# Kernel tuning notes

Hardware: AMD Instinct MI355X
Metric: run time of the kernel (lower is better)

Reference implementation:

```python
import jax, jax.numpy as jnp
import numpy as np

TEMP = 0.1
GROUPS = 16
EPS = 1e-5
COS_EPS = 1e-8


def _encoder(x, conv_w, conv_b, gn_g, gn_b):
    # Conv2d(C,C,3,pad=1) -> GroupNorm(16,C) -> ReLU -> AdaptiveAvgPool2d(1) -> Flatten
    y = jax.lax.conv_general_dilated(
        x, conv_w, window_strides=(1, 1), padding='SAME',
        dimension_numbers=('NCHW', 'OIHW', 'NCHW')) + conv_b[None, :, None, None]
    B, C, H, W = y.shape
    yg = y.reshape(B, GROUPS, C // GROUPS, H, W)
    mu = yg.mean(axis=(2, 3, 4), keepdims=True)
    var = yg.var(axis=(2, 3, 4), keepdims=True)
    yn = ((yg - mu) * jax.lax.rsqrt(var + EPS)).reshape(B, C, H, W)
    y = yn * gn_g[None, :, None, None] + gn_b[None, :, None, None]
    y = jax.nn.relu(y)
    return y.mean(axis=(2, 3))  # [B, C]


def _projector(h, w1, b1, w2, b2, ln_g, ln_b):
    h = jax.nn.relu(h @ w1 + b1)
    h = h @ w2 + b2
    mu = h.mean(axis=-1, keepdims=True)
    var = h.var(axis=-1, keepdims=True)
    return (h - mu) * jax.lax.rsqrt(var + EPS) * ln_g + ln_b


def _predictor(z, w1, b1, w2, b2):
    return jax.nn.relu(z @ w1 + b1) @ w2 + b2


def _l2norm(z):
    n = jnp.sqrt(jnp.sum(z * z, axis=1, keepdims=True))
    return z / jnp.maximum(n, COS_EPS)


def _pair_loss(zi, zj, off_idx):
    # vectorized version of the nested-loop cosine-sim + cross-entropy (label 0)
    S = (_l2norm(zi) @ _l2norm(zj).T) / TEMP  # [B, B]
    pos = jnp.diagonal(S)                     # sim(i_k, j_k)
    neg = jnp.take_along_axis(S, off_idx, axis=1)  # [B, B-1], row k = S[k, l!=k]
    logits = jnp.concatenate([pos[:, None], neg], axis=1)
    return jnp.mean(jax.nn.logsumexp(logits, axis=1) - logits[:, 0])


def setup_inputs() -> dict:
    key = jax.random.key(0)
    ks = jax.random.split(key, 32)
    B, C, H, W, P = 256, 256, 16, 16, 128
    d = {}
    d['x_t2w'] = jax.random.normal(ks[0], (B, C, H, W), jnp.float32)
    d['x_t2f'] = jax.random.normal(ks[1], (B, C, H, W), jnp.float32)
    d['x_t1n'] = jax.random.normal(ks[2], (B, C, H, W), jnp.float32)
    i = 3
    for m in ('t2w', 't2f', 't1n'):
        d[f'conv_w_{m}'] = jax.random.normal(ks[i], (C, C, 3, 3), jnp.float32) * 0.02; i += 1
        d[f'conv_b_{m}'] = jnp.zeros((C,), jnp.float32)
        d[f'gn_g_{m}'] = jnp.ones((C,), jnp.float32)
        d[f'gn_b_{m}'] = jnp.zeros((C,), jnp.float32)
    d['proj_w1'] = jax.random.normal(ks[i], (C, C), jnp.float32) * 0.02; i += 1
    d['proj_b1'] = jnp.zeros((C,), jnp.float32)
    d['proj_w2'] = jax.random.normal(ks[i], (C, P), jnp.float32) * 0.02; i += 1
    d['proj_b2'] = jnp.zeros((P,), jnp.float32)
    d['ln_g'] = jnp.ones((P,), jnp.float32)
    d['ln_b'] = jnp.zeros((P,), jnp.float32)
    d['pred_w1'] = jax.random.normal(ks[i], (P, P), jnp.float32) * 0.02; i += 1
    d['pred_b1'] = jnp.zeros((P,), jnp.float32)
    d['pred_w2'] = jax.random.normal(ks[i], (P, P), jnp.float32) * 0.02; i += 1
    d['pred_b2'] = jnp.zeros((P,), jnp.float32)
    return d


def reference(x_t2w, x_t2f, x_t1n,
              conv_w_t2w, conv_b_t2w, gn_g_t2w, gn_b_t2w,
              conv_w_t2f, conv_b_t2f, gn_g_t2f, gn_b_t2f,
              conv_w_t1n, conv_b_t1n, gn_g_t1n, gn_b_t1n,
              proj_w1, proj_b1, proj_w2, proj_b2, ln_g, ln_b,
              pred_w1, pred_b1, pred_w2, pred_b2):
    xs = [x_t2w, x_t2f, x_t1n]
    enc_params = [(conv_w_t2w, conv_b_t2w, gn_g_t2w, gn_b_t2w),
                  (conv_w_t2f, conv_b_t2f, gn_g_t2f, gn_b_t2f),
                  (conv_w_t1n, conv_b_t1n, gn_g_t1n, gn_b_t1n)]
    encoded = [_encoder(x, *p) for x, p in zip(xs, enc_params)]
    projected = [_projector(e, proj_w1, proj_b1, proj_w2, proj_b2, ln_g, ln_b) for e in encoded]
    preds = [_predictor(z, pred_w1, pred_b1, pred_w2, pred_b2) for z in projected]

    B = projected[0].shape[0]
    off_idx = jnp.asarray(np.array([[l for l in range(B) if l != k] for k in range(B)],
                                    dtype=np.int32))
    pairs = [(0, 1), (0, 2), (1, 2)]
    loss = sum(_pair_loss(projected[i], projected[j], off_idx) for i, j in pairs) / len(pairs)

    return (jnp.stack(encoded), jnp.stack(projected), jnp.stack(preds), loss)
```

## Files before the change

kernel.cpp:

```cpp
#include <hip/hip_runtime.h>
#include <hip/hip_bf16.h>

typedef float f32x4 __attribute__((ext_vector_type(4)));
typedef __bf16 bf16x8 __attribute__((ext_vector_type(8)));
typedef unsigned short u16x8 __attribute__((ext_vector_type(8)));

#define GN_EPS 1e-5f
#define LN_EPS 1e-5f
#define COS_EPS_F 1e-8f

__device__ __forceinline__ unsigned short f2bf(float f) {
  unsigned int u = __builtin_bit_cast(unsigned int, f);
  u += 0x7fffu + ((u >> 16) & 1u);
  return (unsigned short)(u >> 16);
}

__global__ void transpose_kernel(const float* __restrict__ x0,
                                 const float* __restrict__ x1,
                                 const float* __restrict__ x2,
                                 unsigned short* __restrict__ xT,
                                 unsigned int strideElems, int mBase) {
  __shared__ float lds[64][129];
  int m = mBase + (blockIdx.x >> 11);
  int bid = blockIdx.x & 2047;
  const float* x = (m == 0) ? x0 : ((m == 1) ? x1 : x2);
  unsigned short* dst = xT + (unsigned int)(m - mBase) * strideElems;

  int hwt = bid & 3, cit = (bid >> 2) & 1, b = bid >> 3;
  int hw0 = hwt * 64, ci0 = cit * 128;
  int tid = threadIdx.x;

  int hwx = tid & 63, cy0 = tid >> 6;
  const float* xb = x + (b * 256 + ci0) * 256 + hw0;
  #pragma unroll 8
  for (int p = 0; p < 32; ++p) {
    int cy = cy0 + 4 * p;
    lds[hwx][cy] = xb[cy * 256 + hwx];
  }
  __syncthreads();

  int cp = tid & 63, hy0 = tid >> 6;
  unsigned int* outp = (unsigned int*)(dst + (b * 256 + hw0) * 256 + ci0);
  #pragma unroll 4
  for (int p = 0; p < 16; ++p) {
    int hy = hy0 + 4 * p;
    float lo = lds[hy][2 * cp];
    float hi = lds[hy][2 * cp + 1];
    unsigned int w = ((unsigned int)f2bf(hi) << 16) | f2bf(lo);
    outp[hy * 128 + cp] = w;
  }
}

__global__ void pack_kernel(const float* __restrict__ w0,
                            const float* __restrict__ w1,
                            const float* __restrict__ w2,
                            unsigned short* __restrict__ wp,
                            unsigned short* __restrict__ zerobuf) {
  int m = blockIdx.y;
  const float* w = (m == 0) ? w0 : ((m == 1) ? w1 : w2);
  int idx = blockIdx.x * 256 + threadIdx.x;
  if (m == 0 && blockIdx.x == 0 && threadIdx.x < 256) zerobuf[threadIdx.x] = 0;
  int ci = idx & 255;
  int rest = idx >> 8;
  int khw = rest % 9, co = rest / 9;
  wp[m * 589824 + idx] = f2bf(w[(co * 256 + ci) * 9 + khw]);
}

__device__ __forceinline__ void gl_lds16(const unsigned short* g, unsigned short* l) {
  __builtin_amdgcn_global_load_lds(
      (const __attribute__((address_space(1))) void*)g,
      (__attribute__((address_space(3))) void*)l, 16, 0, 0);
}

__launch_bounds__(512, 2)
__global__ void conv_gn_pool(const unsigned short* __restrict__ xT,
                             unsigned int xTstride,
                             const unsigned short* __restrict__ wp,
                             const unsigned short* __restrict__ zb,
                             const float* __restrict__ cb0, const float* __restrict__ cb1,
                             const float* __restrict__ cb2,
                             const float* __restrict__ gg0, const float* __restrict__ gg1,
                             const float* __restrict__ gg2,
                             const float* __restrict__ gb0, const float* __restrict__ gb1,
                             const float* __restrict__ gb2,
                             float* __restrict__ enc, int mBase) {
  __shared__ unsigned short Ab[4][8192];
  __shared__ unsigned short Bb[4][8192];
  __shared__ float gsum[16], gsq[16], pooled[256];

  int mm = mBase + (blockIdx.x >> 8);
  int bb = blockIdx.x & 255;
  int b = (bb & 7) * 32 + (bb >> 3);
  const float* cbias = (mm == 0) ? cb0 : ((mm == 1) ? cb1 : cb2);
  const float* gng   = (mm == 0) ? gg0 : ((mm == 1) ? gg1 : gg2);
  const float* gnb   = (mm == 0) ? gb0 : ((mm == 1) ? gb1 : gb2);

  int tid = threadIdx.x;
  int wid = tid >> 6, lane = tid & 63;
  int wr = wid >> 2, wc = wid & 3;
  int l15 = lane & 15, l4 = lane >> 4;

  if (tid < 16) { gsum[tid] = 0.f; gsq[tid] = 0.f; }
  if (tid < 256) pooled[tid] = 0.f;

  int s0 = tid, s1 = 512 + tid;
  int r0 = s0 >> 2, c0 = s0 & 3;
  int r1 = s1 >> 2, c1 = s1 & 3;
  int cs0 = (c0 ^ ((r0 >> 1) & 3)) * 8;
  int cs1 = (c1 ^ ((r1 >> 1) & 3)) * 8;
  int rh0 = r0 >> 4, rw0 = r0 & 15;
  int rh1 = r1 >> 4, rw1 = r1 & 15;

  const unsigned short* xb = xT + (unsigned int)(mm - mBase) * xTstride + b * 65536;
  const unsigned short* wpm = wp + mm * 589824;
  const unsigned short* bB0 = wpm + r0 * 2304 + cs0;
  const unsigned short* bB1 = wpm + r1 * 2304 + cs1;

  int kch = (l4 ^ ((l15 >> 1) & 3)) * 8;
  int base_af = (wr * 128 + l15) * 32 + kch;
  int base_bf = (wc * 64 + l15) * 32 + kch;

  f32x4 acc[8][4];
  #pragma unroll
  for (int i = 0; i < 8; ++i)
    #pragma unroll
    for (int j = 0; j < 4; ++j) acc[i][j] = (f32x4)(0.0f);

  #define STAGE_A(KC, KHW, BUF)                                                \
    {                                                                          \
      int kh_ = (KHW) / 3, kw_ = (KHW) % 3;                                    \
      int ci0_ = (KC) * 32;                                                    \
      unsigned short* dst_ = &Ab[(BUF)][0];                                    \
      int h0_ = rh0 + kh_ - 1, w0_ = rw0 + kw_ - 1;                            \
      const unsigned short* sA0 = ((unsigned)h0_ < 16u && (unsigned)w0_ < 16u) \
          ? xb + ((h0_ * 16 + w0_) * 256 + ci0_ + cs0) : zb;                   \
      gl_lds16(sA0, dst_ + s0 * 8);                                            \
      int h1_ = rh1 + kh_ - 1, w1_ = rw1 + kw_ - 1;                            \
      const unsigned short* sA1 = ((unsigned)h1_ < 16u && (unsigned)w1_ < 16u) \
          ? xb + ((h1_ * 16 + w1_) * 256 + ci0_ + cs1) : zb;                   \
      gl_lds16(sA1, dst_ + s1 * 8);                                            \
    }
  #define STAGE_B(KC, KHW, BUF)                                                \
    {                                                                          \
      int off_ = (KHW) * 256 + (KC) * 32;                                      \
      unsigned short* dst_ = &Bb[(BUF)][0];                                    \
      gl_lds16(bB0 + off_, dst_ + s0 * 8);                                     \
      gl_lds16(bB1 + off_, dst_ + s1 * 8);                                     \
    }

  #define TILE_COMPUTE(BUF)                                                    \
    {                                                                          \
      const unsigned short* Ap = &Ab[(BUF)][0];                                \
      const unsigned short* Bp = &Bb[(BUF)][0];                                \
      bf16x8 af[8], bfr[4];                                                    \
      _Pragma("unroll")                                                        \
      for (int j = 0; j < 8; ++j)                                              \
        af[j] = __builtin_bit_cast(bf16x8, *(const u16x8*)&Ap[base_af + j * 512]); \
      _Pragma("unroll")                                                        \
      for (int n = 0; n < 4; ++n)                                              \
        bfr[n] = __builtin_bit_cast(bf16x8, *(const u16x8*)&Bp[base_bf + n * 512]); \
      __builtin_amdgcn_s_setprio(1);                                           \
      _Pragma("unroll")                                                        \
      for (int j = 0; j < 8; ++j)                                              \
        _Pragma("unroll")                                                      \
        for (int n = 0; n < 4; ++n)                                            \
          acc[j][n] = __builtin_amdgcn_mfma_f32_16x16x32_bf16(af[j], bfr[n],   \
                                                              acc[j][n], 0, 0, 0); \
      __builtin_amdgcn_s_setprio(0);                                           \
    }

  STAGE_A(0, 0, 0); STAGE_B(0, 0, 0);
  STAGE_A(0, 1, 1); STAGE_B(0, 1, 1);
  STAGE_A(0, 2, 2); STAGE_B(0, 2, 2);
  asm volatile("s_waitcnt vmcnt(8)" ::: "memory");
  __builtin_amdgcn_s_barrier();

  for (int kc = 0; kc < 7; ++kc) {
    #pragma unroll
    for (int khw = 0; khw < 9; ++khw) {
      int buf = (kc + khw) & 3;
      int buf3 = (kc + khw + 3) & 3;
      if (khw <= 5) { STAGE_A(kc, khw + 3, buf3); STAGE_B(kc, khw + 3, buf3); }
      else          { STAGE_A(kc + 1, khw - 6, buf3); STAGE_B(kc + 1, khw - 6, buf3); }
      TILE_COMPUTE(buf);
      asm volatile("s_waitcnt vmcnt(8)" ::: "memory");
      __builtin_amdgcn_s_barrier();
    }
  }
  #pragma unroll
  for (int khw = 0; khw < 9; ++khw) {
    int buf = (7 + khw) & 3;
    int buf3 = (7 + khw + 3) & 3;
    if (khw <= 5) { STAGE_A(7, khw + 3, buf3); STAGE_B(7, khw + 3, buf3); }
    TILE_COMPUTE(buf);
    if (khw <= 5)      asm volatile("s_waitcnt vmcnt(8)" ::: "memory");
    else if (khw == 6) asm volatile("s_waitcnt vmcnt(4)" ::: "memory");
    else               asm volatile("s_waitcnt vmcnt(0)" ::: "memory");
    __builtin_amdgcn_s_barrier();
  }
  #undef STAGE_A
  #undef STAGE_B
  #undef TILE_COMPUTE

  float bias[4], ggv[4], gbv[4];
  #pragma unroll
  for (int nf = 0; nf < 4; ++nf) {
    int co = wc * 64 + nf * 16 + l15;
    bias[nf] = cbias[co]; ggv[nf] = gng[co]; gbv[nf] = gnb[co];
  }
  #pragma unroll
  for (int nf = 0; nf < 4; ++nf) {
    float s1 = 0.f, s2 = 0.f;
    #pragma unroll
    for (int mf = 0; mf < 8; ++mf)
      #pragma unroll
      for (int i = 0; i < 4; ++i) {
        float v = acc[mf][nf][i] + bias[nf];
        acc[mf][nf][i] = v;
        s1 += v; s2 += v * v;
      }
    #pragma unroll
    for (int d = 1; d < 64; d <<= 1) {
      s1 += __shfl_xor(s1, d);
      s2 += __shfl_xor(s2, d);
    }
    if (lane == 0) {
      atomicAdd(&gsum[wc * 4 + nf], s1);
      atomicAdd(&gsq[wc * 4 + nf], s2);
    }
  }
  __syncthreads();
  #pragma unroll
  for (int nf = 0; nf < 4; ++nf) {
    int g = wc * 4 + nf;
    float mean = gsum[g] * (1.f / 4096.f);
    float var = gsq[g] * (1.f / 4096.f) - mean * mean;
    float rs = rsqrtf(var + GN_EPS);
    float p = 0.f;
    #pragma unroll
    for (int mf = 0; mf < 8; ++mf)
      #pragma unroll
      for (int i = 0; i < 4; ++i) {
        float v = (acc[mf][nf][i] - mean) * rs * ggv[nf] + gbv[nf];
        p += fmaxf(v, 0.f);
      }
    p += __shfl_xor(p, 16);
    p += __shfl_xor(p, 32);
    if (lane < 16) atomicAdd(&pooled[wc * 64 + nf * 16 + l15], p);
  }
  __syncthreads();
  if (tid < 256)
    enc[mm * 65536 + b * 256 + tid] = pooled[tid] * (1.f / 256.f);
}

__global__ void proj_pred(const float* __restrict__ enc,
                          const float* __restrict__ w1, const float* __restrict__ b1,
                          const float* __restrict__ w2, const float* __restrict__ b2,
                          const float* __restrict__ lng, const float* __restrict__ lnb,
                          const float* __restrict__ pw1, const float* __restrict__ pb1,
                          const float* __restrict__ pw2, const float* __restrict__ pb2,
                          float* __restrict__ proj, float* __restrict__ pred,
                          float* __restrict__ znorm) {
  __shared__ float row[256], h1[256], zz[128], p1[128], red[2];
  int r = blockIdx.x, tid = threadIdx.x;
  row[tid] = enc[r * 256 + tid];
  __syncthreads();
  float a = 0.f;
  for (int k = 0; k < 256; ++k) a += row[k] * w1[k * 256 + tid];
  h1[tid] = fmaxf(a + b1[tid], 0.f);
  __syncthreads();
  if (tid < 128) {
    a = 0.f;
    for (int k = 0; k < 256; ++k) a += h1[k] * w2[k * 128 + tid];
    zz[tid] = a + b2[tid];
  }
  __syncthreads();
  if (tid == 0) {
    float m = 0.f;
    for (int k = 0; k < 128; ++k) m += zz[k];
    m *= (1.f / 128.f);
    float v = 0.f;
    for (int k = 0; k < 128; ++k) { float d = zz[k] - m; v += d * d; }
    red[0] = m;
    red[1] = rsqrtf(v * (1.f / 128.f) + LN_EPS);
  }
  __syncthreads();
  float zval = 0.f;
  if (tid < 128) {
    zval = (zz[tid] - red[0]) * red[1] * lng[tid] + lnb[tid];
    proj[r * 128 + tid] = zval;
  }
  __syncthreads();
  if (tid < 128) zz[tid] = zval;
  __syncthreads();
  if (tid == 0) {
    float s = 0.f;
    for (int k = 0; k < 128; ++k) s += zz[k] * zz[k];
    red[0] = 1.f / fmaxf(sqrtf(s), COS_EPS_F);
  }
  __syncthreads();
  if (tid < 128) {
    znorm[r * 128 + tid] = zz[tid] * red[0];
    a = 0.f;
    for (int k = 0; k < 128; ++k) a += zz[k] * pw1[k * 128 + tid];
    p1[tid] = fmaxf(a + pb1[tid], 0.f);
  }
  __syncthreads();
  if (tid < 128) {
    a = 0.f;
    for (int k = 0; k < 128; ++k) a += p1[k] * pw2[k * 128 + tid];
    pred[r * 128 + tid] = a + pb2[tid];
  }
}

__global__ void loss_kernel(const float* __restrict__ zn, float* __restrict__ part) {
  __shared__ float zi[128], sv[256], rbuf[256];
  int blk = blockIdx.x;
  int p = blk >> 8, k = blk & 255;
  int i = (p == 2) ? 1 : 0;
  int j = (p == 0) ? 1 : 2;
  int tid = threadIdx.x;
  if (tid < 128) zi[tid] = zn[(i * 256 + k) * 128 + tid];
  __syncthreads();
  const float4* zj = (const float4*)&zn[(j * 256 + tid) * 128];
  float s = 0.f;
  #pragma unroll 8
  for (int d = 0; d < 32; ++d) {
    float4 aq = *(const float4*)&zi[d * 4];
    float4 bq = zj[d];
    s += aq.x * bq.x + aq.y * bq.y + aq.z * bq.z + aq.w * bq.w;
  }
  s *= 10.0f;
  sv[tid] = s;
  rbuf[tid] = s;
  __syncthreads();
  for (int d = 128; d > 0; d >>= 1) {
    if (tid < d) rbuf[tid] = fmaxf(rbuf[tid], rbuf[tid + d]);
    __syncthreads();
  }
  float m = rbuf[0];
  __syncthreads();
  rbuf[tid] = expf(s - m);
  __syncthreads();
  for (int d = 128; d > 0; d >>= 1) {
    if (tid < d) rbuf[tid] += rbuf[tid + d];
    __syncthreads();
  }
  if (tid == 0) part[blk] = m + logf(rbuf[0]) - sv[k];
}

__global__ void finalize_loss(const float* __restrict__ part, float* __restrict__ out) {
  __shared__ float red[256];
  int tid = threadIdx.x;
  float s = 0.f;
  for (int idx = tid; idx < 768; idx += 256) s += part[idx];
  red[tid] = s;
  __syncthreads();
  for (int d = 128; d > 0; d >>= 1) {
    if (tid < d) red[tid] += red[tid + d];
    __syncthreads();
  }
  if (tid == 0) out[0] = red[0] * (1.f / 768.f);
}

extern "C" void kernel_launch(void* const* d_in, const int* in_sizes, int n_in,
                              void* d_out, int out_size, void* d_ws, size_t ws_size,
                              hipStream_t stream) {
  const float* x[3]  = {(const float*)d_in[0], (const float*)d_in[1], (const float*)d_in[2]};
  const float* cw[3] = {(const float*)d_in[3], (const float*)d_in[7], (const float*)d_in[11]};
  const float* cb[3] = {(const float*)d_in[4], (const float*)d_in[8], (const float*)d_in[12]};
  const float* gg[3] = {(const float*)d_in[5], (const float*)d_in[9], (const float*)d_in[13]};
  const float* gb[3] = {(const float*)d_in[6], (const float*)d_in[10], (const float*)d_in[14]};
  const float* p_w1 = (const float*)d_in[15];
  const float* p_b1 = (const float*)d_in[16];
  const float* p_w2 = (const float*)d_in[17];
  const float* p_b2 = (const float*)d_in[18];
  const float* ln_g = (const float*)d_in[19];
  const float* ln_b = (const float*)d_in[20];
  const float* q_w1 = (const float*)d_in[21];
  const float* q_b1 = (const float*)d_in[22];
  const float* q_w2 = (const float*)d_in[23];
  const float* q_b2 = (const float*)d_in[24];

  float* out = (float*)d_out;
  char* ws = (char*)d_ws;

  const size_t XT_ONE = 33554432;
  bool merged = ws_size >= (3 * XT_ONE + 3538944 + 393216 + 3072 + 512);

  size_t xt_total = merged ? 3 * XT_ONE : XT_ONE;
  unsigned short* xT  = (unsigned short*)ws;
  unsigned short* wpk = (unsigned short*)(ws + xt_total);
  float* znorm = (float*)(ws + xt_total + 3538944);
  float* part  = (float*)(ws + xt_total + 3538944 + 393216);
  unsigned short* zb = (unsigned short*)(ws + xt_total + 3538944 + 393216 + 3072);

  float* enc  = out;
  float* proj = out + 196608;
  float* pred = out + 294912;
  float* lossp = out + 393216;

  pack_kernel<<<dim3(2304, 3), dim3(256), 0, stream>>>(cw[0], cw[1], cw[2], wpk, zb);

  if (merged) {
    transpose_kernel<<<dim3(6144), dim3(256), 0, stream>>>(x[0], x[1], x[2], xT, 16777216u, 0);
    conv_gn_pool<<<dim3(768), dim3(512), 0, stream>>>(
        xT, 16777216u, wpk, zb, cb[0], cb[1], cb[2], gg[0], gg[1], gg[2],
        gb[0], gb[1], gb[2], enc, 0);
  } else {
    for (int m = 0; m < 3; ++m) {
      transpose_kernel<<<dim3(2048), dim3(256), 0, stream>>>(x[0], x[1], x[2], xT, 0u, m);
      conv_gn_pool<<<dim3(256), dim3(512), 0, stream>>>(
          xT, 0u, wpk, zb, cb[0], cb[1], cb[2], gg[0], gg[1], gg[2],
          gb[0], gb[1], gb[2], enc, m);
    }
  }
  proj_pred<<<dim3(768), dim3(256), 0, stream>>>(enc, p_w1, p_b1, p_w2, p_b2, ln_g, ln_b,
                                                 q_w1, q_b1, q_w2, q_b2, proj, pred, znorm);
  loss_kernel<<<dim3(768), dim3(256), 0, stream>>>(znorm, part);
  finalize_loss<<<dim3(1), dim3(256), 0, stream>>>(part, lossp);
}
```

Baseline: 330.4 us.

## Software-pipeline LDS fragment loads across K tiles in conv implicit GEMM

```diff
diff --git a/kernel.cpp b/kernel.cpp
--- a/kernel.cpp
+++ b/kernel.cpp
@@ -126,81 +126,95 @@
     #pragma unroll
     for (int j = 0; j < 4; ++j) acc[i][j] = (f32x4)(0.0f);
 
-  #define STAGE_A(KC, KHW, BUF)                                                \
+  int kc3 = 0, kh3 = 0, kw3 = 0;
+
+  #define STAGE(SBUF)                                                          \
     {                                                                          \
-      int kh_ = (KHW) / 3, kw_ = (KHW) % 3;                                    \
-      int ci0_ = (KC) * 32;                                                    \
-      unsigned short* dst_ = &Ab[(BUF)][0];                                    \
-      int h0_ = rh0 + kh_ - 1, w0_ = rw0 + kw_ - 1;                            \
+      int ci0_ = kc3 * 32;                                                     \
+      unsigned short* dstA = &Ab[(SBUF)][0];                                   \
+      int h0_ = rh0 + kh3 - 1, w0_ = rw0 + kw3 - 1;                            \
       const unsigned short* sA0 = ((unsigned)h0_ < 16u && (unsigned)w0_ < 16u) \
           ? xb + ((h0_ * 16 + w0_) * 256 + ci0_ + cs0) : zb;                   \
-      gl_lds16(sA0, dst_ + s0 * 8);                                            \
-      int h1_ = rh1 + kh_ - 1, w1_ = rw1 + kw_ - 1;                            \
+      gl_lds16(sA0, dstA + s0 * 8);                                            \
+      int h1_ = rh1 + kh3 - 1, w1_ = rw1 + kw3 - 1;                            \
       const unsigned short* sA1 = ((unsigned)h1_ < 16u && (unsigned)w1_ < 16u) \
           ? xb + ((h1_ * 16 + w1_) * 256 + ci0_ + cs1) : zb;                   \
-      gl_lds16(sA1, dst_ + s1 * 8);                                            \
+      gl_lds16(sA1, dstA + s1 * 8);                                            \
+      int offB = (kh3 * 3 + kw3) * 256 + ci0_;                                 \
+      unsigned short* dstB = &Bb[(SBUF)][0];                                   \
+      gl_lds16(bB0 + offB, dstB + s0 * 8);                                     \
+      gl_lds16(bB1 + offB, dstB + s1 * 8);                                     \
+      kw3 = kw3 + 1; int cw_ = (kw3 == 3); kw3 = cw_ ? 0 : kw3; kh3 += cw_;    \
+      int ch_ = (kh3 == 3); kh3 = ch_ ? 0 : kh3; kc3 += ch_;                   \
     }
-  #define STAGE_B(KC, KHW, BUF)                                                \
+
+  #define LD8(P) __builtin_bit_cast(bf16x8, *(const u16x8*)(P))
+
+  bf16x8 afA_P[4], afA_Q[4], bfr_P[4], bfr_Q[4], afB[4];
+
+  #define TILE_BODY(BUF, BUF1, SBUF, CUR, NXT, DO_STAGE, VMN, DO_NEXT)         \
     {                                                                          \
-      int off_ = (KHW) * 256 + (KC) * 32;                                      \
-      unsigned short* dst_ = &Bb[(BUF)][0];                                    \
-      gl_lds16(bB0 + off_, dst_ + s0 * 8);                                     \
-      gl_lds16(bB1 + off_, dst_ + s1 * 8);                                     \
-    }
-
-  #define TILE_COMPUTE(BUF)                                                    \
-    {                                                                          \
+      asm volatile("s_waitcnt vmcnt(" #VMN ")" ::: "memory");                  \
+      __builtin_amdgcn_s_barrier();                                            \
+      if (DO_STAGE) STAGE(SBUF);                                               \
       const unsigned short* Ap = &Ab[(BUF)][0];                                \
-      const unsigned short* Bp = &Bb[(BUF)][0];                                \
-      bf16x8 af[8], bfr[4];                                                    \
       _Pragma("unroll")                                                        \
-      for (int j = 0; j < 8; ++j)                                              \
-        af[j] = __builtin_bit_cast(bf16x8, *(const u16x8*)&Ap[base_af + j * 512]); \
-      _Pragma("unroll")                                                        \
-      for (int n = 0; n < 4; ++n)                                              \
-        bfr[n] = __builtin_bit_cast(bf16x8, *(const u16x8*)&Bp[base_bf + n * 512]); \
+      for (int j = 0; j < 4; ++j)                                              \
+        afB[j] = LD8(&Ap[base_af + (4 + j) * 512]);                            \
+      if (DO_NEXT) {                                                           \
+        const unsigned short* Ap1 = &Ab[(BUF1)][0];                            \
+        const unsigned short* Bp1 = &Bb[(BUF1)][0];                            \
+        _Pragma("unroll")                                                      \
+        for (int n = 0; n < 4; ++n)                                            \
+          bfr_##NXT[n] = LD8(&Bp1[base_bf + n * 512]);                         \
+        _Pragma("unroll")                                                      \
+        for (int j = 0; j < 4; ++j)                                            \
+          afA_##NXT[j] = LD8(&Ap1[base_af + j * 512]);                         \
+      }                                                                        \
+      __builtin_amdgcn_sched_barrier(0);                                       \
       __builtin_amdgcn_s_setprio(1);                                           \
       _Pragma("unroll")                                                        \
-      for (int j = 0; j < 8; ++j)                                              \
+      for (int j = 0; j < 4; ++j)                                              \
         _Pragma("unroll")                                                      \
         for (int n = 0; n < 4; ++n)                                            \
-          acc[j][n] = __builtin_amdgcn_mfma_f32_16x16x32_bf16(af[j], bfr[n],   \
-                                                              acc[j][n], 0, 0, 0); \
+          acc[j][n] = __builtin_amdgcn_mfma_f32_16x16x32_bf16(                 \
+              afA_##CUR[j], bfr_##CUR[n], acc[j][n], 0, 0, 0);                 \
+      _Pragma("unroll")                                                        \
+      for (int j = 0; j < 4; ++j)                                              \
+        _Pragma("unroll")                                                      \
+        for (int n = 0; n < 4; ++n)                                            \
+          acc[4 + j][n] = __builtin_amdgcn_mfma_f32_16x16x32_bf16(             \
+              afB[j], bfr_##CUR[n], acc[4 + j][n], 0, 0, 0);                   \
       __builtin_amdgcn_s_setprio(0);                                           \
     }
 
-  STAGE_A(0, 0, 0); STAGE_B(0, 0, 0);
-  STAGE_A(0, 1, 1); STAGE_B(0, 1, 1);
-  STAGE_A(0, 2, 2); STAGE_B(0, 2, 2);
+  STAGE(0); STAGE(1); STAGE(2);
   asm volatile("s_waitcnt vmcnt(8)" ::: "memory");
   __builtin_amdgcn_s_barrier();
-
-  for (int kc = 0; kc < 7; ++kc) {
-    #pragma unroll
-    for (int khw = 0; khw < 9; ++khw) {
-      int buf = (kc + khw) & 3;
-      int buf3 = (kc + khw + 3) & 3;
-      if (khw <= 5) { STAGE_A(kc, khw + 3, buf3); STAGE_B(kc, khw + 3, buf3); }
-      else          { STAGE_A(kc + 1, khw - 6, buf3); STAGE_B(kc + 1, khw - 6, buf3); }
-      TILE_COMPUTE(buf);
-      asm volatile("s_waitcnt vmcnt(8)" ::: "memory");
-      __builtin_amdgcn_s_barrier();
-    }
-  }
-  #pragma unroll
-  for (int khw = 0; khw < 9; ++khw) {
-    int buf = (7 + khw) & 3;
-    int buf3 = (7 + khw + 3) & 3;
-    if (khw <= 5) { STAGE_A(7, khw + 3, buf3); STAGE_B(7, khw + 3, buf3); }
-    TILE_COMPUTE(buf);
-    if (khw <= 5)      asm volatile("s_waitcnt vmcnt(8)" ::: "memory");
-    else if (khw == 6) asm volatile("s_waitcnt vmcnt(4)" ::: "memory");
-    else               asm volatile("s_waitcnt vmcnt(0)" ::: "memory");
-    __builtin_amdgcn_s_barrier();
-  }
-  #undef STAGE_A
-  #undef STAGE_B
-  #undef TILE_COMPUTE
+  {
+    const unsigned short* Ap0 = &Ab[0][0];
+    const unsigned short* Bp0 = &Bb[0][0];
+    #pragma unroll
+    for (int n = 0; n < 4; ++n) bfr_P[n] = LD8(&Bp0[base_bf + n * 512]);
+    #pragma unroll
+    for (int j = 0; j < 4; ++j) afA_P[j] = LD8(&Ap0[base_af + j * 512]);
+  }
+
+  for (int it = 0; it < 17; ++it) {
+    TILE_BODY(0, 1, 3, P, Q, 1, 4, 1);
+    TILE_BODY(1, 2, 0, Q, P, 1, 4, 1);
+    TILE_BODY(2, 3, 1, P, Q, 1, 4, 1);
+    TILE_BODY(3, 0, 2, Q, P, 1, 4, 1);
+  }
+  TILE_BODY(0, 1, 3, P, Q, 1, 4, 1);
+  TILE_BODY(1, 2, 0, Q, P, 0, 4, 1);
+  TILE_BODY(2, 3, 1, P, Q, 0, 0, 1);
+  TILE_BODY(3, 0, 2, Q, P, 0, 0, 0);
+  #undef TILE_BODY
+  #undef STAGE
+  #undef LD8
+
+  __syncthreads();
 
   float bias[4], ggv[4], gbv[4];
   #pragma unroll
```

New measurement: 323.0 us. 2.3% less time.

## Restructure conv tiling to stage input once per channel chunk and shift taps in LDS

Applied to the files above, without the earlier changes.

```diff
diff --git a/kernel.cpp b/kernel.cpp
--- a/kernel.cpp
+++ b/kernel.cpp
@@ -54,12 +54,10 @@
 __global__ void pack_kernel(const float* __restrict__ w0,
                             const float* __restrict__ w1,
                             const float* __restrict__ w2,
-                            unsigned short* __restrict__ wp,
-                            unsigned short* __restrict__ zerobuf) {
+                            unsigned short* __restrict__ wp) {
   int m = blockIdx.y;
   const float* w = (m == 0) ? w0 : ((m == 1) ? w1 : w2);
   int idx = blockIdx.x * 256 + threadIdx.x;
-  if (m == 0 && blockIdx.x == 0 && threadIdx.x < 256) zerobuf[threadIdx.x] = 0;
   int ci = idx & 255;
   int rest = idx >> 8;
   int khw = rest % 9, co = rest / 9;
@@ -76,49 +74,56 @@
 __global__ void conv_gn_pool(const unsigned short* __restrict__ xT,
                              unsigned int xTstride,
                              const unsigned short* __restrict__ wp,
-                             const unsigned short* __restrict__ zb,
                              const float* __restrict__ cb0, const float* __restrict__ cb1,
                              const float* __restrict__ cb2,
                              const float* __restrict__ gg0, const float* __restrict__ gg1,
                              const float* __restrict__ gg2,
                              const float* __restrict__ gb0, const float* __restrict__ gb1,
                              const float* __restrict__ gb2,
-                             float* __restrict__ enc, int mBase) {
-  __shared__ unsigned short Ab[4][8192];
-  __shared__ unsigned short Bb[4][8192];
+                             float* __restrict__ enc, int mBase, int chunk) {
+  __shared__ unsigned short As[2][16384];
+  __shared__ unsigned short Bb[3][4096];
+  __shared__ unsigned short zbuf[32];
   __shared__ float gsum[16], gsq[16], pooled[256];
 
-  int mm = mBase + (blockIdx.x >> 8);
-  int bb = blockIdx.x & 255;
-  int b = (bb & 7) * 32 + (bb >> 3);
+  int bid = blockIdx.x;
+  int xcd = bid & 7, kk = bid >> 3;
+  int nt = kk & 1;
+  int pg = xcd * chunk + (kk >> 1);
+  int mm = mBase + (pg >> 7);
+  int pr = pg & 127;
+
   const float* cbias = (mm == 0) ? cb0 : ((mm == 1) ? cb1 : cb2);
   const float* gng   = (mm == 0) ? gg0 : ((mm == 1) ? gg1 : gg2);
   const float* gnb   = (mm == 0) ? gb0 : ((mm == 1) ? gb1 : gb2);
 
   int tid = threadIdx.x;
   int wid = tid >> 6, lane = tid & 63;
-  int wr = wid >> 2, wc = wid & 3;
+  int wr = wid >> 1, wc = wid & 1;
   int l15 = lane & 15, l4 = lane >> 4;
 
   if (tid < 16) { gsum[tid] = 0.f; gsq[tid] = 0.f; }
   if (tid < 256) pooled[tid] = 0.f;
-
-  int s0 = tid, s1 = 512 + tid;
-  int r0 = s0 >> 2, c0 = s0 & 3;
-  int r1 = s1 >> 2, c1 = s1 & 3;
-  int cs0 = (c0 ^ ((r0 >> 1) & 3)) * 8;
-  int cs1 = (c1 ^ ((r1 >> 1) & 3)) * 8;
-  int rh0 = r0 >> 4, rw0 = r0 & 15;
-  int rh1 = r1 >> 4, rw1 = r1 & 15;
-
-  const unsigned short* xb = xT + (unsigned int)(mm - mBase) * xTstride + b * 65536;
-  const unsigned short* wpm = wp + mm * 589824;
-  const unsigned short* bB0 = wpm + r0 * 2304 + cs0;
-  const unsigned short* bB1 = wpm + r1 * 2304 + cs1;
-
-  int kch = (l4 ^ ((l15 >> 1) & 3)) * 8;
-  int base_af = (wr * 128 + l15) * 32 + kch;
-  int base_bf = (wc * 64 + l15) * 32 + kch;
+  if (tid < 32) zbuf[tid] = 0;
+
+  const unsigned short* xbPair =
+      xT + (unsigned int)(mm - mBase) * xTstride + (unsigned int)(pr * 2) * 65536u;
+  const unsigned short* wpB = wp + mm * 589824 + (nt * 128) * 2304;
+
+  int sco = tid >> 2, sk4 = tid & 3;
+
+  int hh8[8], ww8[8], bq8[8];
+  #pragma unroll
+  for (int mf = 0; mf < 8; ++mf) {
+    int r = wr * 128 + mf * 16 + l15;
+    int img = r >> 8, p = r & 255;
+    hh8[mf] = p >> 4; ww8[mf] = p & 15;
+    bq8[mf] = img * 8192 + p * 32 + l4 * 8;
+  }
+  int bq4[4];
+  #pragma unroll
+  for (int nf = 0; nf < 4; ++nf)
+    bq4[nf] = (wc * 64 + nf * 16 + l15) * 32 + l4 * 8;
 
   f32x4 acc[8][4];
   #pragma unroll
@@ -126,86 +131,103 @@
     #pragma unroll
     for (int j = 0; j < 4; ++j) acc[i][j] = (f32x4)(0.0f);
 
-  #define STAGE_A(KC, KHW, BUF)                                                \
+  #define LD8(P) __builtin_bit_cast(bf16x8, *(const u16x8*)(P))
+
+  #define STAGE_A(KCN, PAR)                                                    \
     {                                                                          \
-      int kh_ = (KHW) / 3, kw_ = (KHW) % 3;                                    \
-      int ci0_ = (KC) * 32;                                                    \
-      unsigned short* dst_ = &Ab[(BUF)][0];                                    \
-      int h0_ = rh0 + kh_ - 1, w0_ = rw0 + kw_ - 1;                            \
-      const unsigned short* sA0 = ((unsigned)h0_ < 16u && (unsigned)w0_ < 16u) \
-          ? xb + ((h0_ * 16 + w0_) * 256 + ci0_ + cs0) : zb;                   \
-      gl_lds16(sA0, dst_ + s0 * 8);                                            \
-      int h1_ = rh1 + kh_ - 1, w1_ = rw1 + kw_ - 1;                            \
-      const unsigned short* sA1 = ((unsigned)h1_ < 16u && (unsigned)w1_ < 16u) \
-          ? xb + ((h1_ * 16 + w1_) * 256 + ci0_ + cs1) : zb;                   \
-      gl_lds16(sA1, dst_ + s1 * 8);                                            \
+      unsigned short* dstA = &As[(PAR)][0];                                    \
+      _Pragma("unroll")                                                        \
+      for (int j = 0; j < 4; ++j) {                                            \
+        int c = tid + j * 512;                                                 \
+        int img_ = c >> 10, p_ = (c >> 2) & 255, k4_ = c & 3;                  \
+        gl_lds16(xbPair + img_ * 65536 + p_ * 256 + (KCN) * 32 + k4_ * 8,      \
+                 dstA + c * 8);                                                \
+      }                                                                        \
     }
-  #define STAGE_B(KC, KHW, BUF)                                                \
+  #define STAGE_B(KC2, TAP2, BUF2)                                             \
+    gl_lds16(wpB + sco * 2304 + (TAP2) * 256 + (KC2) * 32 + sk4 * 8,           \
+             &Bb[(BUF2)][tid * 8]);
+
+  #define TAP_BODY(TAP, DH, DW, DO_A, DO_B, KC2, TAP2, VMN)                    \
     {                                                                          \
-      int off_ = (KHW) * 256 + (KC) * 32;                                      \
-      unsigned short* dst_ = &Bb[(BUF)][0];                                    \
-      gl_lds16(bB0 + off_, dst_ + s0 * 8);                                     \
-      gl_lds16(bB1 + off_, dst_ + s1 * 8);                                     \
-    }
-
-  #define TILE_COMPUTE(BUF)                                                    \
-    {                                                                          \
-      const unsigned short* Ap = &Ab[(BUF)][0];                                \
-      const unsigned short* Bp = &Bb[(BUF)][0];                                \
+      if (DO_A) STAGE_A(kc + 1, (kc + 1) & 1);                                 \
+      if (DO_B) STAGE_B(KC2, TAP2, ((TAP) + 2) % 3);                           \
+      const unsigned short* AsC = &As[kc & 1][0];                              \
       bf16x8 af[8], bfr[4];                                                    \
       _Pragma("unroll")                                                        \
-      for (int j = 0; j < 8; ++j)                                              \
-        af[j] = __builtin_bit_cast(bf16x8, *(const u16x8*)&Ap[base_af + j * 512]); \
+      for (int nf = 0; nf < 4; ++nf)                                           \
+        bfr[nf] = LD8(&Bb[(TAP) % 3][bq4[nf]]);                                \
       _Pragma("unroll")                                                        \
-      for (int n = 0; n < 4; ++n)                                              \
-        bfr[n] = __builtin_bit_cast(bf16x8, *(const u16x8*)&Bp[base_bf + n * 512]); \
+      for (int mf = 0; mf < 8; ++mf) {                                         \
+        int ok = 1;                                                            \
+        if ((DH) == 0) ok &= (hh8[mf] >= 1);                                   \
+        if ((DH) == 2) ok &= (hh8[mf] <= 14);                                  \
+        if ((DW) == 0) ok &= (ww8[mf] >= 1);                                   \
+        if ((DW) == 2) ok &= (ww8[mf] <= 14);                                  \
+        const unsigned short* pa =                                             \
+            ok ? AsC + (bq8[mf] + (((DH) * 16 + (DW)) - 17) * 32)              \
+               : &zbuf[l4 * 8];                                                \
+        af[mf] = LD8(pa);                                                      \
+      }                                                                        \
+      __builtin_amdgcn_s_barrier();                                            \
+      asm volatile("s_waitcnt lgkmcnt(0)" ::: "memory");                       \
+      __builtin_amdgcn_sched_barrier(0);                                       \
       __builtin_amdgcn_s_setprio(1);                                           \
       _Pragma("unroll")                                                        \
-      for (int j = 0; j < 8; ++j)                                              \
+      for (int mf = 0; mf < 8; ++mf)                                           \
         _Pragma("unroll")                                                      \
-        for (int n = 0; n < 4; ++n)                                            \
-          acc[j][n] = __builtin_amdgcn_mfma_f32_16x16x32_bf16(af[j], bfr[n],   \
-                                                              acc[j][n], 0, 0, 0); \
+        for (int nf = 0; nf < 4; ++nf)                                         \
+          acc[mf][nf] = __builtin_amdgcn_mfma_f32_16x16x32_bf16(               \
+              af[mf], bfr[nf], acc[mf][nf], 0, 0, 0);                          \
       __builtin_amdgcn_s_setprio(0);                                           \
+      asm volatile("s_waitcnt vmcnt(" #VMN ")" ::: "memory");                  \
+      __builtin_amdgcn_s_barrier();                                            \
     }
 
-  STAGE_A(0, 0, 0); STAGE_B(0, 0, 0);
-  STAGE_A(0, 1, 1); STAGE_B(0, 1, 1);
-  STAGE_A(0, 2, 2); STAGE_B(0, 2, 2);
-  asm volatile("s_waitcnt vmcnt(8)" ::: "memory");
-  __builtin_amdgcn_s_barrier();
+  {
+    int kc = 0; (void)kc;
+    STAGE_A(0, 0);
+    STAGE_B(0, 0, 0);
+    STAGE_B(0, 1, 1);
+    asm volatile("s_waitcnt vmcnt(1)" ::: "memory");
+    __builtin_amdgcn_s_barrier();
+  }
 
   for (int kc = 0; kc < 7; ++kc) {
-    #pragma unroll
-    for (int khw = 0; khw < 9; ++khw) {
-      int buf = (kc + khw) & 3;
-      int buf3 = (kc + khw + 3) & 3;
-      if (khw <= 5) { STAGE_A(kc, khw + 3, buf3); STAGE_B(kc, khw + 3, buf3); }
-      else          { STAGE_A(kc + 1, khw - 6, buf3); STAGE_B(kc + 1, khw - 6, buf3); }
-      TILE_COMPUTE(buf);
-      asm volatile("s_waitcnt vmcnt(8)" ::: "memory");
-      __builtin_amdgcn_s_barrier();
-    }
-  }
-  #pragma unroll
-  for (int khw = 0; khw < 9; ++khw) {
-    int buf = (7 + khw) & 3;
-    int buf3 = (7 + khw + 3) & 3;
-    if (khw <= 5) { STAGE_A(7, khw + 3, buf3); STAGE_B(7, khw + 3, buf3); }
-    TILE_COMPUTE(buf);
-    if (khw <= 5)      asm volatile("s_waitcnt vmcnt(8)" ::: "memory");
-    else if (khw == 6) asm volatile("s_waitcnt vmcnt(4)" ::: "memory");
-    else               asm volatile("s_waitcnt vmcnt(0)" ::: "memory");
-    __builtin_amdgcn_s_barrier();
-  }
+    TAP_BODY(0, 0, 0, 1, 1, kc, 2, 5)
+    TAP_BODY(1, 0, 1, 0, 1, kc, 3, 1)
+    TAP_BODY(2, 0, 2, 0, 1, kc, 4, 1)
+    TAP_BODY(3, 1, 0, 0, 1, kc, 5, 1)
+    TAP_BODY(4, 1, 1, 0, 1, kc, 6, 1)
+    TAP_BODY(5, 1, 2, 0, 1, kc, 7, 1)
+    TAP_BODY(6, 2, 0, 0, 1, kc, 8, 1)
+    TAP_BODY(7, 2, 1, 0, 1, kc + 1, 0, 1)
+    TAP_BODY(8, 2, 2, 0, 1, kc + 1, 1, 1)
+  }
+  {
+    const int kc = 7;
+    TAP_BODY(0, 0, 0, 0, 1, 7, 2, 1)
+    TAP_BODY(1, 0, 1, 0, 1, 7, 3, 1)
+    TAP_BODY(2, 0, 2, 0, 1, 7, 4, 1)
+    TAP_BODY(3, 1, 0, 0, 1, 7, 5, 1)
+    TAP_BODY(4, 1, 1, 0, 1, 7, 6, 1)
+    TAP_BODY(5, 1, 2, 0, 1, 7, 7, 1)
+    TAP_BODY(6, 2, 0, 0, 1, 7, 8, 1)
+    TAP_BODY(7, 2, 1, 0, 0, 7, 0, 0)
+    TAP_BODY(8, 2, 2, 0, 0, 7, 0, 0)
+  }
+  #undef TAP_BODY
   #undef STAGE_A
   #undef STAGE_B
-  #undef TILE_COMPUTE
-
+  #undef LD8
+
+  __syncthreads();
+
+  int img = wr >> 1;
   float bias[4], ggv[4], gbv[4];
   #pragma unroll
   for (int nf = 0; nf < 4; ++nf) {
-    int co = wc * 64 + nf * 16 + l15;
+    int co = nt * 128 + wc * 64 + nf * 16 + l15;
     bias[nf] = cbias[co]; ggv[nf] = gng[co]; gbv[nf] = gnb[co];
   }
   #pragma unroll
@@ -225,14 +247,14 @@
       s2 += __shfl_xor(s2, d);
     }
     if (lane == 0) {
-      atomicAdd(&gsum[wc * 4 + nf], s1);
-      atomicAdd(&gsq[wc * 4 + nf], s2);
+      atomicAdd(&gsum[img * 8 + wc * 4 + nf], s1);
+      atomicAdd(&gsq[img * 8 + wc * 4 + nf], s2);
     }
   }
   __syncthreads();
   #pragma unroll
   for (int nf = 0; nf < 4; ++nf) {
-    int g = wc * 4 + nf;
+    int g = img * 8 + wc * 4 + nf;
     float mean = gsum[g] * (1.f / 4096.f);
     float var = gsq[g] * (1.f / 4096.f) - mean * mean;
     float rs = rsqrtf(var + GN_EPS);
@@ -246,11 +268,14 @@
       }
     p += __shfl_xor(p, 16);
     p += __shfl_xor(p, 32);
-    if (lane < 16) atomicAdd(&pooled[wc * 64 + nf * 16 + l15], p);
-  }
-  __syncthreads();
-  if (tid < 256)
-    enc[mm * 65536 + b * 256 + tid] = pooled[tid] * (1.f / 256.f);
+    if (lane < 16) atomicAdd(&pooled[img * 128 + wc * 64 + nf * 16 + l15], p);
+  }
+  __syncthreads();
+  if (tid < 256) {
+    int oimg = tid >> 7, ch = tid & 127;
+    enc[mm * 65536 + (pr * 2 + oimg) * 256 + nt * 128 + ch] =
+        pooled[tid] * (1.f / 256.f);
+  }
 }
 
 __global__ void proj_pred(const float* __restrict__ enc,
@@ -393,26 +418,25 @@
   unsigned short* wpk = (unsigned short*)(ws + xt_total);
   float* znorm = (float*)(ws + xt_total + 3538944);
   float* part  = (float*)(ws + xt_total + 3538944 + 393216);
-  unsigned short* zb = (unsigned short*)(ws + xt_total + 3538944 + 393216 + 3072);
 
   float* enc  = out;
   float* proj = out + 196608;
   float* pred = out + 294912;
   float* lossp = out + 393216;
 
-  pack_kernel<<<dim3(2304, 3), dim3(256), 0, stream>>>(cw[0], cw[1], cw[2], wpk, zb);
+  pack_kernel<<<dim3(2304, 3), dim3(256), 0, stream>>>(cw[0], cw[1], cw[2], wpk);
 
   if (merged) {
     transpose_kernel<<<dim3(6144), dim3(256), 0, stream>>>(x[0], x[1], x[2], xT, 16777216u, 0);
     conv_gn_pool<<<dim3(768), dim3(512), 0, stream>>>(
-        xT, 16777216u, wpk, zb, cb[0], cb[1], cb[2], gg[0], gg[1], gg[2],
-        gb[0], gb[1], gb[2], enc, 0);
+        xT, 16777216u, wpk, cb[0], cb[1], cb[2], gg[0], gg[1], gg[2],
+        gb[0], gb[1], gb[2], enc, 0, 48);
   } else {
     for (int m = 0; m < 3; ++m) {
       transpose_kernel<<<dim3(2048), dim3(256), 0, stream>>>(x[0], x[1], x[2], xT, 0u, m);
       conv_gn_pool<<<dim3(256), dim3(512), 0, stream>>>(
-          xT, 0u, wpk, zb, cb[0], cb[1], cb[2], gg[0], gg[1], gg[2],
-          gb[0], gb[1], gb[2], enc, m);
+          xT, 0u, wpk, cb[0], cb[1], cb[2], gg[0], gg[1], gg[2],
+          gb[0], gb[1], gb[2], enc, m, 16);
     }
   }
   proj_pred<<<dim3(768), dim3(256), 0, stream>>>(enc, p_w1, p_b1, p_w2, p_b2, ln_g, ln_b,
```

After: 343.9 us. 4.1% more time.
